# Kernel tuning notes

Hardware: AMD Instinct MI355X
Metric: run time of the kernel (lower is better)

## Reference

```python
import jax, jax.numpy as jnp
import numpy as np

B, S, D, H = 2, 2048, 1024, 16
DH = D // H
EPS = 1e-5


def setup_inputs() -> dict:
    key = jax.random.key(0)
    ks = jax.random.split(key, 12)
    inp = {
        "Q_source": jax.random.normal(ks[0], (B, S, D), jnp.float32),
        "K_source": jax.random.normal(ks[1], (B, S, D), jnp.float32),
        "V_source": jax.random.normal(ks[2], (B, S, D), jnp.float32),
        "padding_mask": jnp.zeros((B, 1, 1, S), dtype=bool),  # no padded keys (avoids NaN rows)
        "future_mask": jnp.triu(jnp.ones((S, S), dtype=bool), k=1)[None, None],  # causal
    }
    sc = 1.0 / np.sqrt(D)
    names = ["WQ", "WK", "WV", "WO"]
    for i, n in enumerate(names):
        inp[n] = jax.random.normal(ks[3 + i], (D, D), jnp.float32) * sc
        inp["b" + n[1]] = jnp.zeros((D,), jnp.float32)
    inp["gamma"] = jnp.ones((D,), jnp.float32)
    inp["beta"] = jnp.zeros((D,), jnp.float32)
    return inp


def reference(Q_source, K_source, V_source, padding_mask, future_mask,
              WQ, bQ, WK, bK, WV, bV, WO, bO, gamma, beta):
    b = Q_source.shape[0]
    # torch Linear: x @ W.T + b ; reshape to [B, H, S, DH]
    def proj(x, W, bb):
        y = x @ W.T + bb
        return y.reshape(b, -1, H, DH).transpose(0, 2, 1, 3)

    Q = proj(Q_source, WQ, bQ)
    K = proj(K_source, WK, bK)
    V = proj(V_source, WV, bV)

    scores = jnp.einsum("bhqd,bhkd->bhqk", Q, K) / jnp.sqrt(jnp.float32(DH))
    neg_inf = jnp.float32(-jnp.inf)
    scores = jnp.where(padding_mask, neg_inf, scores)
    scores = jnp.where(future_mask, neg_inf, scores)
    attn = jax.nn.softmax(scores, axis=-1)

    ctx = jnp.einsum("bhqk,bhkd->bhqd", attn, V)
    ctx = ctx.transpose(0, 2, 1, 3).reshape(b, -1, D)
    out = ctx @ WO.T + bO

    x = Q_source + out
    mu = x.mean(-1, keepdims=True)
    var = x.var(-1, keepdims=True)
    return (x - mu) * jax.lax.rsqrt(var + EPS) * gamma + beta
```

## Files before the change

### kernel.cpp

```cpp
#include <hip/hip_runtime.h>

#define S_LEN 2048
#define DMODEL 1024
#define NH 16
#define DHD 64

typedef __attribute__((ext_vector_type(8))) short bh8;
typedef __attribute__((ext_vector_type(4))) float f32x4;
typedef __attribute__((ext_vector_type(2))) unsigned int u32x2;
typedef __attribute__((ext_vector_type(4))) unsigned int u32x4;
typedef unsigned short u16;
typedef unsigned int u32;

static __device__ __forceinline__ u16 f2bf(float f) {
    unsigned u = __builtin_bit_cast(unsigned, f);
    u += 0x7fffu + ((u >> 16) & 1u);
    return (u16)(u >> 16);
}

typedef const __attribute__((address_space(1))) void* gptr_t;
typedef __attribute__((address_space(3))) void* lptr_t;

static __device__ __forceinline__ void gll16(const void* g, void* l) {
    __builtin_amdgcn_global_load_lds((gptr_t)g, (lptr_t)l, 16, 0, 0);
}

__global__ __launch_bounds__(256) void cvt_all(const float* __restrict__ WQ, const float* __restrict__ WK,
                                               const float* __restrict__ WV, const float* __restrict__ WO,
                                               const float* __restrict__ S0, const float* __restrict__ S1,
                                               const float* __restrict__ S2,
                                               u16* __restrict__ wq, u16* __restrict__ wk,
                                               u16* __restrict__ wv, u16* __restrict__ wo,
                                               u16* __restrict__ q0, u16* __restrict__ k0,
                                               u16* __restrict__ v0) {
    int bid = blockIdx.x;
    const float* s;
    u16* o;
    size_t base;
    if (bid < 2048) {
        int wi = bid >> 9;
        s = wi == 0 ? WQ : (wi == 1 ? WK : (wi == 2 ? WV : WO));
        o = wi == 0 ? wq : (wi == 1 ? wk : (wi == 2 ? wv : wo));
        base = (size_t)(bid & 511) * 2048;
    } else {
        int r = bid - 2048;
        int si = r >> 11;
        s = si == 0 ? S0 : (si == 1 ? S1 : S2);
        o = si == 0 ? q0 : (si == 1 ? k0 : v0);
        base = (size_t)(r & 2047) * 2048;
    }
    size_t i = base + (size_t)threadIdx.x * 8;
    float4 a = *(const float4*)(s + i);
    float4 b = *(const float4*)(s + i + 4);
    u32 p0 = (u32)f2bf(a.x) | ((u32)f2bf(a.y) << 16);
    u32 p1 = (u32)f2bf(a.z) | ((u32)f2bf(a.w) << 16);
    u32 p2 = (u32)f2bf(b.x) | ((u32)f2bf(b.y) << 16);
    u32 p3 = (u32)f2bf(b.z) | ((u32)f2bf(b.w) << 16);
    *(u32x4*)(o + i) = (u32x4){p0, p1, p2, p3};
}

template <int BM, int OBF, int AF32>
static __device__ __forceinline__ void gemm_body(const void* __restrict__ Ap, const u16* __restrict__ Bm,
                                                 const float* __restrict__ bias, void* __restrict__ Cv,
                                                 int N, int K, int bi, int bj, short* Al, short* Bl,
                                                 float oscale) {
    constexpr int MI = BM / 32;
    constexpr int NC = BM / 64;
    int tid = threadIdx.x, lane = tid & 63, w = tid >> 6;
    int ln = lane & 15, hi = lane >> 4;
    int wm = w >> 1, wn = w & 1;
    f32x4 acc[MI][4];
#pragma unroll
    for (int i = 0; i < MI; i++)
#pragma unroll
        for (int j = 0; j < 4; j++) acc[i][j] = (f32x4){0.f, 0.f, 0.f, 0.f};
    int nk = K >> 5;

    float4 fa[NC][2];
    auto loadA = [&](int kt) {
#pragma unroll
        for (int c = 0; c < NC; ++c) {
            int o = c * 4096 + tid * 16;
            int row = o >> 6, e0 = (o & 63) >> 1;
            const float* src = (const float*)Ap + (size_t)(bi * BM + row) * K + kt * 32 + e0;
            fa[c][0] = *(const float4*)src;
            fa[c][1] = *(const float4*)(src + 4);
        }
    };
    auto writeA = [&](int buf) {
#pragma unroll
        for (int c = 0; c < NC; ++c) {
            int o = c * 4096 + tid * 16;
            u32 w0 = (u32)f2bf(fa[c][0].x) | ((u32)f2bf(fa[c][0].y) << 16);
            u32 w1 = (u32)f2bf(fa[c][0].z) | ((u32)f2bf(fa[c][0].w) << 16);
            u32 w2 = (u32)f2bf(fa[c][1].x) | ((u32)f2bf(fa[c][1].y) << 16);
            u32 w3 = (u32)f2bf(fa[c][1].z) | ((u32)f2bf(fa[c][1].w) << 16);
            *(u32x4*)((char*)(Al + buf * (BM * 32)) + o) = (u32x4){w0, w1, w2, w3};
        }
    };
    auto stageA_lds = [&](int buf, int kt) {
#pragma unroll
        for (int c = 0; c < NC; ++c) {
            int o = c * 4096 + tid * 16;
            int row = o >> 6, col = (o & 63) >> 1;
            gll16((const u16*)Ap + (size_t)(bi * BM + row) * K + kt * 32 + col,
                  (char*)(Al + buf * (BM * 32)) + o);
        }
    };
    auto stageB = [&](int buf, int kt) {
#pragma unroll
        for (int c = 0; c < 2; ++c) {
            int o = c * 4096 + tid * 16;
            int row = o >> 6, col = (o & 63) >> 1;
            gll16(Bm + (size_t)(bj * 128 + row) * K + kt * 32 + col, (char*)(Bl + buf * 4096) + o);
        }
    };

    if constexpr (AF32) { loadA(0); writeA(0); } else { stageA_lds(0, 0); }
    stageB(0, 0);
    __syncthreads();
    int cur = 0;
    for (int kt = 0; kt < nk; ++kt) {
        bool pre = (kt + 1 < nk);
        if (pre) {
            if constexpr (AF32) loadA(kt + 1); else stageA_lds(cur ^ 1, kt + 1);
            stageB(cur ^ 1, kt + 1);
        }
        bh8 av[MI], bv[4];
#pragma unroll
        for (int i = 0; i < MI; i++) av[i] = *(const bh8*)&Al[cur * (BM * 32) + (wm * (BM / 2) + i * 16 + ln) * 32 + hi * 8];
#pragma unroll
        for (int j = 0; j < 4; j++) bv[j] = *(const bh8*)&Bl[cur * 4096 + (wn * 64 + j * 16 + ln) * 32 + hi * 8];
#pragma unroll
        for (int i = 0; i < MI; i++)
#pragma unroll
            for (int j = 0; j < 4; j++)
                acc[i][j] = __builtin_amdgcn_mfma_f32_16x16x32_bf16(av[i], bv[j], acc[i][j], 0, 0, 0);
        if constexpr (AF32) { if (pre) writeA(cur ^ 1); }
        __syncthreads();
        cur ^= 1;
    }
    if constexpr (OBF == 2) {
#pragma unroll
        for (int j = 0; j < 4; j++) {
            int col = wn * 64 + j * 16 + ln;
            float bvs = bias[bj * 128 + col];
#pragma unroll
            for (int i = 0; i < MI; i++) {
                int row0 = wm * (BM / 2) + i * 16 + hi * 4;
                u32 p01 = (u32)f2bf(acc[i][j][0] + bvs) | ((u32)f2bf(acc[i][j][1] + bvs) << 16);
                u32 p23 = (u32)f2bf(acc[i][j][2] + bvs) | ((u32)f2bf(acc[i][j][3] + bvs) << 16);
                int idx = col * 128 + (row0 ^ ((col & 7) << 3));
                *(u32x2*)&Al[idx] = (u32x2){p01, p23};
            }
        }
        __syncthreads();
        int b = bi >> 4;
        int sbase = (bi & 15) * 128;
#pragma unroll
        for (int it = 0; it < 8; ++it) {
            int idx = it * 256 + tid;
            int dcol = idx >> 4;
            int sl = (idx & 15) * 8;
            bh8 v = *(const bh8*)&Al[dcol * 128 + (sl ^ ((dcol & 7) << 3))];
            int h = bj * 2 + (dcol >> 6), d = dcol & 63;
            *(bh8*)((u16*)Cv + ((size_t)((b * 16 + h) * 64 + d)) * 2048 + sbase + sl) = v;
        }
        return;
    }
#pragma unroll
    for (int j = 0; j < 4; j++) {
        int col = bj * 128 + wn * 64 + j * 16 + ln;
        float bvs = bias[col];
#pragma unroll
        for (int i = 0; i < MI; i++) {
            int row0 = bi * BM + wm * (BM / 2) + i * 16 + hi * 4;
#pragma unroll
            for (int rr = 0; rr < 4; rr++) {
                if (OBF) {
                    float v = (acc[i][j][rr] + bvs) * oscale;
                    ((u16*)Cv)[(size_t)(row0 + rr) * N + col] = f2bf(v);
                } else {
                    ((float*)Cv)[(size_t)(row0 + rr) * N + col] = acc[i][j][rr] + bvs;
                }
            }
        }
    }
}

__global__ __launch_bounds__(256, 3) void gemm_qkv(const u16* __restrict__ A0, const u16* __restrict__ A1,
                                                   const u16* __restrict__ A2, const u16* __restrict__ B0,
                                                   const u16* __restrict__ B1, const u16* __restrict__ B2,
                                                   const float* __restrict__ c0, const float* __restrict__ c1,
                                                   const float* __restrict__ c2, u16* __restrict__ C0,
                                                   u16* __restrict__ C1, u16* __restrict__ VT) {
    __shared__ short SH[16384];
    short* Al = SH;
    short* Bl = SH + 8192;
    int bid = blockIdx.x;
    int swz = (bid & 7) * 96 + (bid >> 3);
    int z = swz >> 8, t = swz & 255;
    if (z == 2) {
        gemm_body<128, 2, 0>(A2, B2, c2, VT, 1024, 1024, t >> 3, t & 7, Al, Bl, 1.0f);
    } else if (z == 0) {
        gemm_body<128, 1, 0>(A0, B0, c0, C0, 1024, 1024, t >> 3, t & 7, Al, Bl, 0.18033688f);
    } else {
        gemm_body<128, 1, 0>(A1, B1, c1, C1, 1024, 1024, t >> 3, t & 7, Al, Bl, 1.0f);
    }
}

__global__ __launch_bounds__(256) void gemm_o(const u16* __restrict__ A, const u16* __restrict__ Bm,
                                              const float* __restrict__ bias, float* __restrict__ C) {
    __shared__ short Al[2 * 64 * 32];
    __shared__ short Bl[2 * 128 * 32];
    int bid = blockIdx.x;
    int swz = (bid & 7) * 64 + (bid >> 3);
    gemm_body<64, 0, 0>(A, Bm, bias, C, 1024, 1024, swz >> 3, swz & 7, Al, Bl, 1.0f);
}

template <int PLO, int PHI>
static __device__ __forceinline__ void attn_core(const u16* __restrict__ Qp, const u16* __restrict__ Kp,
                                                 const u16* __restrict__ VT, u16* __restrict__ Ctx,
                                                 short* Klb, short* Vlb, short* Pw,
                                                 int b, int h, int bh, int qt, int tid) {
    int lane = tid & 63, w = tid >> 6;
    int ln = lane & 15, hi = lane >> 4;
    __builtin_amdgcn_s_setprio(PLO);
    bh8 ones;
#pragma unroll
    for (int e = 0; e < 8; e++) ones[e] = (short)0x3F80;

    auto stage_kv = [&](int buf, int kt) {
#pragma unroll
        for (int c = 0; c < 2; ++c) {
            int o = c * 4096 + tid * 16;
            int r = o >> 7;
            int slot = (o >> 4) & 7;
            gll16(Kp + ((size_t)(b * S_LEN + kt * 64 + r)) * DMODEL + h * DHD + ((slot ^ (r & 7)) << 3),
                  (char*)(Klb + buf * 4096) + o);
            gll16(VT + ((size_t)(bh * DHD + r)) * S_LEN + kt * 64 + ((slot ^ (r & 7)) << 3),
                  (char*)(Vlb + buf * 4096) + o);
        }
    };

    int nt = 2 * qt + 2;
    int qg0 = (qt << 7) + w * 32 + ln;
    const bh8* qr0 = (const bh8*)(Qp + ((size_t)(b * S_LEN + qg0)) * DMODEL + h * DHD);
    const bh8* qr1 = (const bh8*)(Qp + ((size_t)(b * S_LEN + qg0 + 16)) * DMODEL + h * DHD);
    bh8 qf[2][2];
    qf[0][0] = qr0[hi]; qf[0][1] = qr0[4 + hi];
    qf[1][0] = qr1[hi]; qf[1][1] = qr1[4 + hi];
    f32x4 ctxa[2][4];
    f32x4 lacc[2];
#pragma unroll
    for (int g = 0; g < 2; g++) {
        lacc[g] = (f32x4){0.f, 0.f, 0.f, 0.f};
#pragma unroll
        for (int i = 0; i < 4; i++) ctxa[g][i] = (f32x4){0.f, 0.f, 0.f, 0.f};
    }
    stage_kv(0, 0);
    __syncthreads();
    int cur = 0;
    for (int kt = 0; kt < nt; ++kt) {
        if (kt + 1 < nt) stage_kv(cur ^ 1, kt + 1);
        f32x4 sc[2][4];
#pragma unroll
        for (int g = 0; g < 2; g++)
#pragma unroll
            for (int ks = 0; ks < 4; ++ks) sc[g][ks] = (f32x4){0.f, 0.f, 0.f, 0.f};
        __builtin_amdgcn_s_setprio(PHI);
#pragma unroll
        for (int dwin = 0; dwin < 2; ++dwin) {
#pragma unroll
            for (int ks = 0; ks < 4; ++ks) {
                int r = ks * 16 + ln;
                bh8 kv = *(const bh8*)&Klb[cur * 4096 + r * 64 + ((dwin * 32 + hi * 8) ^ ((r & 7) << 3))];
                sc[0][ks] = __builtin_amdgcn_mfma_f32_16x16x32_bf16(kv, qf[0][dwin], sc[0][ks], 0, 0, 0);
                sc[1][ks] = __builtin_amdgcn_mfma_f32_16x16x32_bf16(kv, qf[1][dwin], sc[1][ks], 0, 0, 0);
            }
        }
        __builtin_amdgcn_s_setprio(PLO);
        if (kt >= nt - 2) {
#pragma unroll
            for (int g = 0; g < 2; g++) {
                int qgq = qg0 + g * 16;
#pragma unroll
                for (int ks = 0; ks < 4; ++ks)
#pragma unroll
                    for (int rr = 0; rr < 4; ++rr) {
                        int kg = kt * 64 + ks * 16 + hi * 4 + rr;
                        sc[g][ks][rr] = (kg <= qgq) ? sc[g][ks][rr] : -1e30f;
                    }
            }
        }
#pragma unroll
        for (int g = 0; g < 2; g++) {
#pragma unroll
            for (int ks = 0; ks < 4; ++ks) {
                u32 u0 = __builtin_bit_cast(u32, __builtin_amdgcn_exp2f(sc[g][ks][0]));
                u32 u1 = __builtin_bit_cast(u32, __builtin_amdgcn_exp2f(sc[g][ks][1]));
                u32 u2 = __builtin_bit_cast(u32, __builtin_amdgcn_exp2f(sc[g][ks][2]));
                u32 u3 = __builtin_bit_cast(u32, __builtin_amdgcn_exp2f(sc[g][ks][3]));
                u32 a01 = (u0 >> 16) | (u1 & 0xffff0000u);
                u32 a23 = (u2 >> 16) | (u3 & 0xffff0000u);
                int kloc = ks * 16 + hi * 4;
                *(u32x2*)&Pw[(g * 16 + ln) * 64 + (kloc ^ ((ln & 7) << 3))] = (u32x2){a01, a23};
            }
        }
        __builtin_amdgcn_s_setprio(PHI);
#pragma unroll
        for (int kw = 0; kw < 2; ++kw) {
            bh8 pf0 = *(const bh8*)&Pw[ln * 64 + ((kw * 32 + hi * 8) ^ ((ln & 7) << 3))];
            bh8 pf1 = *(const bh8*)&Pw[(16 + ln) * 64 + ((kw * 32 + hi * 8) ^ ((ln & 7) << 3))];
            lacc[0] = __builtin_amdgcn_mfma_f32_16x16x32_bf16(ones, pf0, lacc[0], 0, 0, 0);
            lacc[1] = __builtin_amdgcn_mfma_f32_16x16x32_bf16(ones, pf1, lacc[1], 0, 0, 0);
#pragma unroll
            for (int ds = 0; ds < 4; ++ds) {
                int d = ds * 16 + ln;
                bh8 vf = *(const bh8*)&Vlb[cur * 4096 + d * 64 + ((kw * 32 + hi * 8) ^ ((d & 7) << 3))];
                ctxa[0][ds] = __builtin_amdgcn_mfma_f32_16x16x32_bf16(vf, pf0, ctxa[0][ds], 0, 0, 0);
                ctxa[1][ds] = __builtin_amdgcn_mfma_f32_16x16x32_bf16(vf, pf1, ctxa[1][ds], 0, 0, 0);
            }
        }
        __builtin_amdgcn_s_setprio(PLO);
        __syncthreads();
        cur ^= 1;
    }
#pragma unroll
    for (int g = 0; g < 2; g++) {
        float inv = 1.f / lacc[g][0];
        u16* cp = Ctx + ((size_t)(b * S_LEN + qg0 + g * 16)) * DMODEL + h * DHD;
#pragma unroll
        for (int ds = 0; ds < 4; ++ds) {
            ushort4 st;
            st.x = f2bf(ctxa[g][ds][0] * inv);
            st.y = f2bf(ctxa[g][ds][1] * inv);
            st.z = f2bf(ctxa[g][ds][2] * inv);
            st.w = f2bf(ctxa[g][ds][3] * inv);
            *(ushort4*)(cp + ds * 16 + hi * 4) = st;
        }
    }
    __builtin_amdgcn_s_setprio(0);
}

__global__ __launch_bounds__(256, 2) void attn_fwd(const u16* __restrict__ Qp, const u16* __restrict__ Kp,
                                                   const u16* __restrict__ VT, u16* __restrict__ Ctx) {
    __shared__ short Kl[2][64 * 64];
    __shared__ short Vl[2][64 * 64];
    __shared__ short Pl[4][32 * 64];
    int tid = threadIdx.x, w = tid >> 6;
    int bid = blockIdx.x;
    int xcd = bid & 7, j = bid >> 3;
    int rnd = j >> 5, cu = j & 31;
    int bh = xcd * 4 + rnd * 2 + (cu >> 4);
    int qtl = cu & 15;
    int qt = rnd ? (15 - qtl) : qtl;
    int b = bh >> 4, h = bh & 15;
    if (qt >= 8)
        attn_core<2, 3>(Qp, Kp, VT, Ctx, &Kl[0][0], &Vl[0][0], &Pl[w][0], b, h, bh, qt, tid);
    else
        attn_core<0, 1>(Qp, Kp, VT, Ctx, &Kl[0][0], &Vl[0][0], &Pl[w][0], b, h, bh, qt, tid);
}

__global__ __launch_bounds__(256) void ln_res(const float* __restrict__ Xres, const float* __restrict__ Y,
                                              const float* __restrict__ gamma, const float* __restrict__ beta,
                                              float* __restrict__ out) {
    int row = blockIdx.x, tid = threadIdx.x;
    const float4* xr = (const float4*)(Xres + (size_t)row * DMODEL);
    const float4* yr = (const float4*)(Y + (size_t)row * DMODEL);
    float4 a = xr[tid], bq = yr[tid];
    float x0 = a.x + bq.x, x1 = a.y + bq.y, x2 = a.z + bq.z, x3 = a.w + bq.w;
    float s1 = x0 + x1 + x2 + x3;
    float s2 = x0 * x0 + x1 * x1 + x2 * x2 + x3 * x3;
#pragma unroll
    for (int off = 32; off > 0; off >>= 1) {
        s1 += __shfl_xor(s1, off);
        s2 += __shfl_xor(s2, off);
    }
    __shared__ float r1[4], r2[4];
    int wv = tid >> 6;
    if ((tid & 63) == 0) { r1[wv] = s1; r2[wv] = s2; }
    __syncthreads();
    s1 = r1[0] + r1[1] + r1[2] + r1[3];
    s2 = r2[0] + r2[1] + r2[2] + r2[3];
    float mu = s1 * (1.0f / 1024.0f);
    float var = s2 * (1.0f / 1024.0f) - mu * mu;
    float rstd = rsqrtf(var + 1e-5f);
    const float4* g4 = (const float4*)gamma;
    const float4* b4 = (const float4*)beta;
    float4 g = g4[tid], bb = b4[tid];
    float4 res;
    res.x = (x0 - mu) * rstd * g.x + bb.x;
    res.y = (x1 - mu) * rstd * g.y + bb.y;
    res.z = (x2 - mu) * rstd * g.z + bb.z;
    res.w = (x3 - mu) * rstd * g.w + bb.w;
    *((float4*)(out + (size_t)row * DMODEL) + tid) = res;
}

extern "C" void kernel_launch(void* const* d_in, const int* in_sizes, int n_in,
                              void* d_out, int out_size, void* d_ws, size_t ws_size,
                              hipStream_t stream) {
    const float* Qs = (const float*)d_in[0];
    const float* Ks = (const float*)d_in[1];
    const float* Vs = (const float*)d_in[2];
    const float* WQ = (const float*)d_in[5];
    const float* bQ = (const float*)d_in[6];
    const float* WK = (const float*)d_in[7];
    const float* bK = (const float*)d_in[8];
    const float* WV = (const float*)d_in[9];
    const float* bV = (const float*)d_in[10];
    const float* WO = (const float*)d_in[11];
    const float* bO = (const float*)d_in[12];
    const float* gamma = (const float*)d_in[13];
    const float* beta = (const float*)d_in[14];

    const size_t MB = 1u << 20;
    char* w8 = (char*)d_ws;
    u16* Qb  = (u16*)(w8 + 0 * MB);
    u16* Kb  = (u16*)(w8 + 8 * MB);
    u16* Vb  = (u16*)(w8 + 16 * MB);
    u16* WQb = (u16*)(w8 + 24 * MB);
    u16* WKb = (u16*)(w8 + 26 * MB);
    u16* WVb = (u16*)(w8 + 28 * MB);
    u16* WOb = (u16*)(w8 + 30 * MB);
    u16* Qp  = (u16*)(w8 + 32 * MB);
    u16* Kp  = (u16*)(w8 + 40 * MB);
    u16* VTb = (u16*)(w8 + 56 * MB);
    u16* Ctx = (u16*)(w8 + 64 * MB);
    float* Y2 = (float*)(w8 + 72 * MB);

    cvt_all<<<8192, 256, 0, stream>>>(WQ, WK, WV, WO, Qs, Ks, Vs, WQb, WKb, WVb, WOb, Qb, Kb, Vb);
    gemm_qkv<<<768, 256, 0, stream>>>(Qb, Kb, Vb, WQb, WKb, WVb, bQ, bK, bV, Qp, Kp, VTb);
    attn_fwd<<<512, 256, 0, stream>>>(Qp, Kp, VTb, Ctx);
    gemm_o<<<512, 256, 0, stream>>>(Ctx, WOb, bO, Y2);
    ln_res<<<4096, 256, 0, stream>>>(Qs, Y2, gamma, beta, (float*)d_out);
}
```

Before: 119.2 us.

## Split long causal attention tiles across two KV chunks with atomic-counter merge

Query tiles in the upper half of the causal range now have their KV loop split into two chunks handled by separate blocks. Each block writes unnormalised fp32 partial context and row sums to workspace, and the last block to finish (found with an atomic counter) sums and normalises them. This removes the load imbalance where long tiles dominate the tail. The grid grows from 512 to 768 blocks, occupancy is raised to 3 blocks per CU, and the per-tile setprio templating is dropped. The cost is extra global traffic for the partials, an atomic per tile, and a counter reset in the convert kernel. Merging by plain sum is valid only because this kernel never subtracts a running max before exp2.

```diff
diff --git a/kernel.cpp b/kernel.cpp
--- a/kernel.cpp
+++ b/kernel.cpp
@@ -32,8 +32,9 @@
                                                u16* __restrict__ wq, u16* __restrict__ wk,
                                                u16* __restrict__ wv, u16* __restrict__ wo,
                                                u16* __restrict__ q0, u16* __restrict__ k0,
-                                               u16* __restrict__ v0) {
+                                               u16* __restrict__ v0, u32* __restrict__ cnt) {
     int bid = blockIdx.x;
+    if (bid == 0) cnt[threadIdx.x] = 0u;
     const float* s;
     u16* o;
     size_t base;
@@ -218,14 +219,30 @@
     gemm_body<64, 0, 0>(A, Bm, bias, C, 1024, 1024, swz >> 3, swz & 7, Al, Bl, 1.0f);
 }
 
-template <int PLO, int PHI>
-static __device__ __forceinline__ void attn_core(const u16* __restrict__ Qp, const u16* __restrict__ Kp,
-                                                 const u16* __restrict__ VT, u16* __restrict__ Ctx,
-                                                 short* Klb, short* Vlb, short* Pw,
-                                                 int b, int h, int bh, int qt, int tid) {
-    int lane = tid & 63, w = tid >> 6;
+__global__ __launch_bounds__(256, 3) void attn_fwd(const u16* __restrict__ Qp, const u16* __restrict__ Kp,
+                                                   const u16* __restrict__ VT, u16* __restrict__ Ctx,
+                                                   float* __restrict__ Part, float* __restrict__ Lp,
+                                                   u32* __restrict__ Cnt) {
+    __shared__ short Kl[2][4096];
+    __shared__ short Vl[2][4096];
+    __shared__ short Pl[4][2048];
+    __shared__ int redflag;
+    int tid = threadIdx.x, lane = tid & 63, w = tid >> 6;
     int ln = lane & 15, hi = lane >> 4;
-    __builtin_amdgcn_s_setprio(PLO);
+    int bid = blockIdx.x;
+    int xcd = bid & 7, r = bid >> 3;
+    int bh = xcd * 4 + (r & 3);
+    int j24 = r >> 2;
+    int qt, ch;
+    if (j24 < 8)       { qt = 8 + j24;  ch = 0; }
+    else if (j24 < 16) { qt = 23 - j24; ch = 1; }
+    else               { qt = j24 - 16; ch = 0; }
+    int nc = (qt >= 8) ? 2 : 1;
+    int nt = 2 * qt + 2;
+    int kbeg = ch * 16;
+    int kend = (ch == nc - 1) ? nt : 16;
+    int b = bh >> 4, h = bh & 15;
+    short* Pw = &Pl[w][0];
     bh8 ones;
 #pragma unroll
     for (int e = 0; e < 8; e++) ones[e] = (short)0x3F80;
@@ -234,16 +251,15 @@
 #pragma unroll
         for (int c = 0; c < 2; ++c) {
             int o = c * 4096 + tid * 16;
-            int r = o >> 7;
+            int rr = o >> 7;
             int slot = (o >> 4) & 7;
-            gll16(Kp + ((size_t)(b * S_LEN + kt * 64 + r)) * DMODEL + h * DHD + ((slot ^ (r & 7)) << 3),
-                  (char*)(Klb + buf * 4096) + o);
-            gll16(VT + ((size_t)(bh * DHD + r)) * S_LEN + kt * 64 + ((slot ^ (r & 7)) << 3),
-                  (char*)(Vlb + buf * 4096) + o);
+            gll16(Kp + ((size_t)(b * S_LEN + kt * 64 + rr)) * DMODEL + h * DHD + ((slot ^ (rr & 7)) << 3),
+                  (char*)(&Kl[buf][0]) + o);
+            gll16(VT + ((size_t)(bh * DHD + rr)) * S_LEN + kt * 64 + ((slot ^ (rr & 7)) << 3),
+                  (char*)(&Vl[buf][0]) + o);
         }
     };
 
-    int nt = 2 * qt + 2;
     int qg0 = (qt << 7) + w * 32 + ln;
     const bh8* qr0 = (const bh8*)(Qp + ((size_t)(b * S_LEN + qg0)) * DMODEL + h * DHD);
     const bh8* qr1 = (const bh8*)(Qp + ((size_t)(b * S_LEN + qg0 + 16)) * DMODEL + h * DHD);
@@ -258,28 +274,28 @@
 #pragma unroll
         for (int i = 0; i < 4; i++) ctxa[g][i] = (f32x4){0.f, 0.f, 0.f, 0.f};
     }
-    stage_kv(0, 0);
+    stage_kv(0, kbeg);
     __syncthreads();
     int cur = 0;
-    for (int kt = 0; kt < nt; ++kt) {
-        if (kt + 1 < nt) stage_kv(cur ^ 1, kt + 1);
+    for (int kt = kbeg; kt < kend; ++kt) {
+        if (kt + 1 < kend) stage_kv(cur ^ 1, kt + 1);
         f32x4 sc[2][4];
 #pragma unroll
         for (int g = 0; g < 2; g++)
 #pragma unroll
             for (int ks = 0; ks < 4; ++ks) sc[g][ks] = (f32x4){0.f, 0.f, 0.f, 0.f};
-        __builtin_amdgcn_s_setprio(PHI);
+        __builtin_amdgcn_s_setprio(1);
 #pragma unroll
         for (int dwin = 0; dwin < 2; ++dwin) {
 #pragma unroll
             for (int ks = 0; ks < 4; ++ks) {
-                int r = ks * 16 + ln;
-                bh8 kv = *(const bh8*)&Klb[cur * 4096 + r * 64 + ((dwin * 32 + hi * 8) ^ ((r & 7) << 3))];
+                int rr = ks * 16 + ln;
+                bh8 kv = *(const bh8*)&Kl[cur][rr * 64 + ((dwin * 32 + hi * 8) ^ ((rr & 7) << 3))];
                 sc[0][ks] = __builtin_amdgcn_mfma_f32_16x16x32_bf16(kv, qf[0][dwin], sc[0][ks], 0, 0, 0);
                 sc[1][ks] = __builtin_amdgcn_mfma_f32_16x16x32_bf16(kv, qf[1][dwin], sc[1][ks], 0, 0, 0);
             }
         }
-        __builtin_amdgcn_s_setprio(PLO);
+        __builtin_amdgcn_s_setprio(0);
         if (kt >= nt - 2) {
 #pragma unroll
             for (int g = 0; g < 2; g++) {
@@ -307,7 +323,7 @@
                 *(u32x2*)&Pw[(g * 16 + ln) * 64 + (kloc ^ ((ln & 7) << 3))] = (u32x2){a01, a23};
             }
         }
-        __builtin_amdgcn_s_setprio(PHI);
+        __builtin_amdgcn_s_setprio(1);
 #pragma unroll
         for (int kw = 0; kw < 2; ++kw) {
             bh8 pf0 = *(const bh8*)&Pw[ln * 64 + ((kw * 32 + hi * 8) ^ ((ln & 7) << 3))];
@@ -317,49 +333,71 @@
 #pragma unroll
             for (int ds = 0; ds < 4; ++ds) {
                 int d = ds * 16 + ln;
-                bh8 vf = *(const bh8*)&Vlb[cur * 4096 + d * 64 + ((kw * 32 + hi * 8) ^ ((d & 7) << 3))];
+                bh8 vf = *(const bh8*)&Vl[cur][d * 64 + ((kw * 32 + hi * 8) ^ ((d & 7) << 3))];
                 ctxa[0][ds] = __builtin_amdgcn_mfma_f32_16x16x32_bf16(vf, pf0, ctxa[0][ds], 0, 0, 0);
                 ctxa[1][ds] = __builtin_amdgcn_mfma_f32_16x16x32_bf16(vf, pf1, ctxa[1][ds], 0, 0, 0);
             }
         }
-        __builtin_amdgcn_s_setprio(PLO);
+        __builtin_amdgcn_s_setprio(0);
         __syncthreads();
         cur ^= 1;
     }
+
+    if (nc == 1) {
+#pragma unroll
+        for (int g = 0; g < 2; g++) {
+            float inv = 1.f / lacc[g][0];
+            u16* cp = Ctx + ((size_t)(b * S_LEN + qg0 + g * 16)) * DMODEL + h * DHD;
+#pragma unroll
+            for (int ds = 0; ds < 4; ++ds) {
+                ushort4 st;
+                st.x = f2bf(ctxa[g][ds][0] * inv);
+                st.y = f2bf(ctxa[g][ds][1] * inv);
+                st.z = f2bf(ctxa[g][ds][2] * inv);
+                st.w = f2bf(ctxa[g][ds][3] * inv);
+                *(ushort4*)(cp + ds * 16 + hi * 4) = st;
+            }
+        }
+        return;
+    }
+    int ptile = bh * 8 + (qt - 8);
+    float* Pb = Part + ((size_t)ptile * 2 + ch) * (128 * 64);
+    float* Lb = Lp + ((size_t)ptile * 2 + ch) * 128;
 #pragma unroll
     for (int g = 0; g < 2; g++) {
-        float inv = 1.f / lacc[g][0];
-        u16* cp = Ctx + ((size_t)(b * S_LEN + qg0 + g * 16)) * DMODEL + h * DHD;
+        int qloc = w * 32 + g * 16 + ln;
 #pragma unroll
         for (int ds = 0; ds < 4; ++ds) {
+            *(f32x4*)&Pb[qloc * 64 + ds * 16 + hi * 4] = ctxa[g][ds];
+        }
+        if (hi == 0) Lb[qloc] = lacc[g][0];
+    }
+    __syncthreads();
+    __threadfence();
+    if (tid == 0) redflag = (atomicAdd(&Cnt[ptile], 1u) == (u32)(nc - 1)) ? 1 : 0;
+    __syncthreads();
+    if (redflag) {
+        __threadfence();
+        const float* P0 = Part + ((size_t)ptile * 2 + 0) * (128 * 64);
+        const float* P1 = Part + ((size_t)ptile * 2 + 1) * (128 * 64);
+        const float* L0 = Lp + ((size_t)ptile * 2 + 0) * 128;
+        const float* L1 = Lp + ((size_t)ptile * 2 + 1) * 128;
+#pragma unroll
+        for (int it = 0; it < 8; ++it) {
+            int idx = it * 256 + tid;
+            int q = idx >> 4;
+            int d4 = (idx & 15) * 4;
+            f32x4 a = *(const f32x4*)&P0[q * 64 + d4];
+            f32x4 c2 = *(const f32x4*)&P1[q * 64 + d4];
+            float invl = 1.f / (L0[q] + L1[q]);
             ushort4 st;
-            st.x = f2bf(ctxa[g][ds][0] * inv);
-            st.y = f2bf(ctxa[g][ds][1] * inv);
-            st.z = f2bf(ctxa[g][ds][2] * inv);
-            st.w = f2bf(ctxa[g][ds][3] * inv);
-            *(ushort4*)(cp + ds * 16 + hi * 4) = st;
-        }
-    }
-    __builtin_amdgcn_s_setprio(0);
-}
-
-__global__ __launch_bounds__(256, 2) void attn_fwd(const u16* __restrict__ Qp, const u16* __restrict__ Kp,
-                                                   const u16* __restrict__ VT, u16* __restrict__ Ctx) {
-    __shared__ short Kl[2][64 * 64];
-    __shared__ short Vl[2][64 * 64];
-    __shared__ short Pl[4][32 * 64];
-    int tid = threadIdx.x, w = tid >> 6;
-    int bid = blockIdx.x;
-    int xcd = bid & 7, j = bid >> 3;
-    int rnd = j >> 5, cu = j & 31;
-    int bh = xcd * 4 + rnd * 2 + (cu >> 4);
-    int qtl = cu & 15;
-    int qt = rnd ? (15 - qtl) : qtl;
-    int b = bh >> 4, h = bh & 15;
-    if (qt >= 8)
-        attn_core<2, 3>(Qp, Kp, VT, Ctx, &Kl[0][0], &Vl[0][0], &Pl[w][0], b, h, bh, qt, tid);
-    else
-        attn_core<0, 1>(Qp, Kp, VT, Ctx, &Kl[0][0], &Vl[0][0], &Pl[w][0], b, h, bh, qt, tid);
+            st.x = f2bf((a[0] + c2[0]) * invl);
+            st.y = f2bf((a[1] + c2[1]) * invl);
+            st.z = f2bf((a[2] + c2[2]) * invl);
+            st.w = f2bf((a[3] + c2[3]) * invl);
+            *(ushort4*)(Ctx + ((size_t)(b * S_LEN + (qt << 7) + q)) * DMODEL + h * DHD + d4) = st;
+        }
+    }
 }
 
 __global__ __launch_bounds__(256) void ln_res(const float* __restrict__ Xres, const float* __restrict__ Y,
@@ -428,10 +466,13 @@
     u16* VTb = (u16*)(w8 + 56 * MB);
     u16* Ctx = (u16*)(w8 + 64 * MB);
     float* Y2 = (float*)(w8 + 72 * MB);
-
-    cvt_all<<<8192, 256, 0, stream>>>(WQ, WK, WV, WO, Qs, Ks, Vs, WQb, WKb, WVb, WOb, Qb, Kb, Vb);
+    float* Part = (float*)(w8 + 88 * MB);
+    float* Lpart = (float*)(w8 + 104 * MB);
+    u32* Cnt = (u32*)(w8 + 105 * MB);
+
+    cvt_all<<<8192, 256, 0, stream>>>(WQ, WK, WV, WO, Qs, Ks, Vs, WQb, WKb, WVb, WOb, Qb, Kb, Vb, Cnt);
     gemm_qkv<<<768, 256, 0, stream>>>(Qb, Kb, Vb, WQb, WKb, WVb, bQ, bK, bV, Qp, Kp, VTb);
-    attn_fwd<<<512, 256, 0, stream>>>(Qp, Kp, VTb, Ctx);
+    attn_fwd<<<768, 256, 0, stream>>>(Qp, Kp, VTb, Ctx, Part, Lpart, Cnt);
     gemm_o<<<512, 256, 0, stream>>>(Ctx, WOb, bO, Y2);
     ln_res<<<4096, 256, 0, stream>>>(Qs, Y2, gamma, beta, (float*)d_out);
 }
```

After: 200.6 us. 1.68x slower.

## Split causal KV loop across two wave groups and merge partial contexts

Applied to the files above, without the earlier changes.

The attention kernel now launches 512-thread blocks in which two groups of four waves each handle half of the key/value tiles for the same 128-query tile. Each group has its own double-buffered K/V staging. At the end, group 1 writes its partial context and row sums to shared memory, reusing the K buffer, and group 0 adds them, normalizes and stores. This halves the serial KV loop per block and changes the block-to-tile mapping to balance causal work, which should shorten the tail of long tiles. The cost is an extra shared-memory reduction and barrier, and one block per CU instead of two.

```diff
diff --git a/kernel.cpp b/kernel.cpp
--- a/kernel.cpp
+++ b/kernel.cpp
@@ -221,9 +221,12 @@
 template <int PLO, int PHI>
 static __device__ __forceinline__ void attn_core(const u16* __restrict__ Qp, const u16* __restrict__ Kp,
                                                  const u16* __restrict__ VT, u16* __restrict__ Ctx,
-                                                 short* Klb, short* Vlb, short* Pw,
+                                                 short* Klb, short* Vlb, short* Pw, float* Csh, float* Ls,
                                                  int b, int h, int bh, int qt, int tid) {
     int lane = tid & 63, w = tid >> 6;
+    int grp = w >> 2;
+    int qsub = w & 3;
+    int tgl = tid & 255;
     int ln = lane & 15, hi = lane >> 4;
     __builtin_amdgcn_s_setprio(PLO);
     bh8 ones;
@@ -233,18 +236,20 @@
     auto stage_kv = [&](int buf, int kt) {
 #pragma unroll
         for (int c = 0; c < 2; ++c) {
-            int o = c * 4096 + tid * 16;
-            int r = o >> 7;
+            int o = c * 4096 + tgl * 16;
+            int rr = o >> 7;
             int slot = (o >> 4) & 7;
-            gll16(Kp + ((size_t)(b * S_LEN + kt * 64 + r)) * DMODEL + h * DHD + ((slot ^ (r & 7)) << 3),
+            gll16(Kp + ((size_t)(b * S_LEN + kt * 64 + rr)) * DMODEL + h * DHD + ((slot ^ (rr & 7)) << 3),
                   (char*)(Klb + buf * 4096) + o);
-            gll16(VT + ((size_t)(bh * DHD + r)) * S_LEN + kt * 64 + ((slot ^ (r & 7)) << 3),
+            gll16(VT + ((size_t)(bh * DHD + rr)) * S_LEN + kt * 64 + ((slot ^ (rr & 7)) << 3),
                   (char*)(Vlb + buf * 4096) + o);
         }
     };
 
+    int nh = qt + 1;
     int nt = 2 * qt + 2;
-    int qg0 = (qt << 7) + w * 32 + ln;
+    int kbase = grp * nh;
+    int qg0 = (qt << 7) + qsub * 32 + ln;
     const bh8* qr0 = (const bh8*)(Qp + ((size_t)(b * S_LEN + qg0)) * DMODEL + h * DHD);
     const bh8* qr1 = (const bh8*)(Qp + ((size_t)(b * S_LEN + qg0 + 16)) * DMODEL + h * DHD);
     bh8 qf[2][2];
@@ -258,11 +263,12 @@
 #pragma unroll
         for (int i = 0; i < 4; i++) ctxa[g][i] = (f32x4){0.f, 0.f, 0.f, 0.f};
     }
-    stage_kv(0, 0);
+    stage_kv(0, kbase);
     __syncthreads();
     int cur = 0;
-    for (int kt = 0; kt < nt; ++kt) {
-        if (kt + 1 < nt) stage_kv(cur ^ 1, kt + 1);
+    for (int i = 0; i < nh; ++i) {
+        int kt = kbase + i;
+        if (i + 1 < nh) stage_kv(cur ^ 1, kt + 1);
         f32x4 sc[2][4];
 #pragma unroll
         for (int g = 0; g < 2; g++)
@@ -273,8 +279,8 @@
         for (int dwin = 0; dwin < 2; ++dwin) {
 #pragma unroll
             for (int ks = 0; ks < 4; ++ks) {
-                int r = ks * 16 + ln;
-                bh8 kv = *(const bh8*)&Klb[cur * 4096 + r * 64 + ((dwin * 32 + hi * 8) ^ ((r & 7) << 3))];
+                int rr = ks * 16 + ln;
+                bh8 kv = *(const bh8*)&Klb[cur * 4096 + rr * 64 + ((dwin * 32 + hi * 8) ^ ((rr & 7) << 3))];
                 sc[0][ks] = __builtin_amdgcn_mfma_f32_16x16x32_bf16(kv, qf[0][dwin], sc[0][ks], 0, 0, 0);
                 sc[1][ks] = __builtin_amdgcn_mfma_f32_16x16x32_bf16(kv, qf[1][dwin], sc[1][ks], 0, 0, 0);
             }
@@ -326,40 +332,61 @@
         __syncthreads();
         cur ^= 1;
     }
-#pragma unroll
-    for (int g = 0; g < 2; g++) {
-        float inv = 1.f / lacc[g][0];
-        u16* cp = Ctx + ((size_t)(b * S_LEN + qg0 + g * 16)) * DMODEL + h * DHD;
-#pragma unroll
-        for (int ds = 0; ds < 4; ++ds) {
-            ushort4 st;
-            st.x = f2bf(ctxa[g][ds][0] * inv);
-            st.y = f2bf(ctxa[g][ds][1] * inv);
-            st.z = f2bf(ctxa[g][ds][2] * inv);
-            st.w = f2bf(ctxa[g][ds][3] * inv);
-            *(ushort4*)(cp + ds * 16 + hi * 4) = st;
-        }
-    }
     __builtin_amdgcn_s_setprio(0);
-}
-
-__global__ __launch_bounds__(256, 2) void attn_fwd(const u16* __restrict__ Qp, const u16* __restrict__ Kp,
+    if (grp == 1) {
+#pragma unroll
+        for (int g = 0; g < 2; g++) {
+            int qloc = g * 16 + ln;
+#pragma unroll
+            for (int ds = 0; ds < 4; ++ds) {
+                int doff = (ds * 16 + hi * 4) ^ ((qloc & 7) << 3);
+                *(f32x4*)&Csh[(qsub * 32 + qloc) * 64 + doff] = ctxa[g][ds];
+            }
+            if (hi == 0) Ls[qsub * 32 + qloc] = lacc[g][0];
+        }
+    }
+    __syncthreads();
+    if (grp == 0) {
+#pragma unroll
+        for (int g = 0; g < 2; g++) {
+            int qloc = g * 16 + ln;
+            float inv = 1.f / (lacc[g][0] + Ls[qsub * 32 + qloc]);
+            u16* cp = Ctx + ((size_t)(b * S_LEN + qg0 + g * 16)) * DMODEL + h * DHD;
+#pragma unroll
+            for (int ds = 0; ds < 4; ++ds) {
+                int doff = (ds * 16 + hi * 4) ^ ((qloc & 7) << 3);
+                f32x4 p = *(const f32x4*)&Csh[(qsub * 32 + qloc) * 64 + doff];
+                ushort4 st;
+                st.x = f2bf((ctxa[g][ds][0] + p[0]) * inv);
+                st.y = f2bf((ctxa[g][ds][1] + p[1]) * inv);
+                st.z = f2bf((ctxa[g][ds][2] + p[2]) * inv);
+                st.w = f2bf((ctxa[g][ds][3] + p[3]) * inv);
+                *(ushort4*)(cp + ds * 16 + hi * 4) = st;
+            }
+        }
+    }
+}
+
+__global__ __launch_bounds__(512, 1) void attn_fwd(const u16* __restrict__ Qp, const u16* __restrict__ Kp,
                                                    const u16* __restrict__ VT, u16* __restrict__ Ctx) {
-    __shared__ short Kl[2][64 * 64];
-    __shared__ short Vl[2][64 * 64];
-    __shared__ short Pl[4][32 * 64];
+    __shared__ short Kl[2][2][4096];
+    __shared__ short Vl[2][2][4096];
+    __shared__ short Pl[8][2048];
+    __shared__ float Ls[128];
     int tid = threadIdx.x, w = tid >> 6;
+    int grp = w >> 2;
     int bid = blockIdx.x;
-    int xcd = bid & 7, j = bid >> 3;
-    int rnd = j >> 5, cu = j & 31;
-    int bh = xcd * 4 + rnd * 2 + (cu >> 4);
-    int qtl = cu & 15;
-    int qt = rnd ? (15 - qtl) : qtl;
+    int rnd = bid >> 8, slot = bid & 255;
+    int xcd = slot & 7, t = slot >> 3;
+    int bh = xcd * 4 + (t & 3);
+    int qte = t >> 2;
+    int qt = rnd ? (15 - 2 * qte) : (2 * qte);
     int b = bh >> 4, h = bh & 15;
+    float* Csh = (float*)&Kl[0][0][0];
     if (qt >= 8)
-        attn_core<2, 3>(Qp, Kp, VT, Ctx, &Kl[0][0], &Vl[0][0], &Pl[w][0], b, h, bh, qt, tid);
+        attn_core<2, 3>(Qp, Kp, VT, Ctx, &Kl[grp][0][0], &Vl[grp][0][0], &Pl[w][0], Csh, Ls, b, h, bh, qt, tid);
     else
-        attn_core<0, 1>(Qp, Kp, VT, Ctx, &Kl[0][0], &Vl[0][0], &Pl[w][0], b, h, bh, qt, tid);
+        attn_core<0, 1>(Qp, Kp, VT, Ctx, &Kl[grp][0][0], &Vl[grp][0][0], &Pl[w][0], Csh, Ls, b, h, bh, qt, tid);
 }
 
 __global__ __launch_bounds__(256) void ln_res(const float* __restrict__ Xres, const float* __restrict__ Y,
@@ -431,7 +458,7 @@
 
     cvt_all<<<8192, 256, 0, stream>>>(WQ, WK, WV, WO, Qs, Ks, Vs, WQb, WKb, WVb, WOb, Qb, Kb, Vb);
     gemm_qkv<<<768, 256, 0, stream>>>(Qb, Kb, Vb, WQb, WKb, WVb, bQ, bK, bV, Qp, Kp, VTb);
-    attn_fwd<<<512, 256, 0, stream>>>(Qp, Kp, VTb, Ctx);
+    attn_fwd<<<512, 512, 0, stream>>>(Qp, Kp, VTb, Ctx);
     gemm_o<<<512, 256, 0, stream>>>(Ctx, WOb, bO, Y2);
     ln_res<<<4096, 256, 0, stream>>>(Qs, Y2, gamma, beta, (float*)d_out);
 }
```

After: 112.9 us. 5.3% less time.
